# Kernel tuning notes

Measured on AMD Instinct MI355X. Metric: run time of the kernel, lower is better.

## Reference

```python
import jax, jax.numpy as jnp
import numpy as np

B, S, D_MODEL, D_POL = 2048, 64, 768, 64
SCALE = 1.0 / np.sqrt(D_POL).astype(np.float32)  # 1/sqrt(policy_d) = 0.125


def mish(x):
    return x * jnp.tanh(jax.nn.softplus(x))


def setup_inputs() -> dict:
    key = jax.random.key(0)
    ks = jax.random.split(key, 10)
    s = lambda fan: 1.0 / np.sqrt(fan)
    return {
        "x": jax.random.normal(ks[0], (B, S, D_MODEL), dtype=jnp.float32),
        "W1": jax.random.normal(ks[1], (D_MODEL, D_MODEL), dtype=jnp.float32) * s(D_MODEL),
        "b1": jax.random.normal(ks[2], (D_MODEL,), dtype=jnp.float32) * 0.01,
        "Wq": jax.random.normal(ks[3], (D_MODEL, D_POL), dtype=jnp.float32) * s(D_MODEL),
        "bq": jax.random.normal(ks[4], (D_POL,), dtype=jnp.float32) * 0.01,
        "Wk": jax.random.normal(ks[5], (D_MODEL, D_POL), dtype=jnp.float32) * s(D_MODEL),
        "bk": jax.random.normal(ks[6], (D_POL,), dtype=jnp.float32) * 0.01,
        "Wp": jax.random.normal(ks[7], (D_POL, 4), dtype=jnp.float32) * s(D_POL),
        "bp": jax.random.normal(ks[8], (4,), dtype=jnp.float32) * 0.01,
        "indices": jax.random.randint(ks[9], (1858,), 0, 4288, dtype=jnp.int64 if jax.config.read("jax_enable_x64") else jnp.int32),
    }


def reference(x, W1, b1, Wq, bq, Wk, bk, Wp, bp, indices):
    b = x.shape[0]
    h = mish(x @ W1 + b1)                      # [B,64,768] dense1 + mish
    q = h @ Wq + bq                            # [B,64,64]
    k = h @ Wk + bk                            # [B,64,64]
    scores = jnp.einsum("bqd,bkd->bqk", q, k) * SCALE  # [B,64,64]
    # promotion head on 8th-rank keys: Linear(D_POL -> 4)
    prom = k[:, 56:64, :] @ Wp + bp            # [B,8,4]
    # transpose/split[3,1]/add/transpose == add 4th channel to first 3
    prom = prom[:, :, :3] + prom[:, :, 3:4]    # [B,8,3]
    prom = prom.reshape(b, 1, 24)
    s2 = scores[:, 48:56, 56:64].reshape(b, 64, 1)
    s2 = jnp.concatenate([s2, s2, s2], axis=-1).reshape(b, 8, 24)
    promotion = (s2 + prom).reshape(b, 3, 64)  # [B,3,64]
    policy = jnp.concatenate([scores, promotion], axis=1).reshape(b, 4288)
    return policy[:, indices]                  # [B,1858]
```

## Files before the change

### kernel.cpp

```cpp
#include <hip/hip_runtime.h>

typedef __attribute__((ext_vector_type(8))) short short8;
typedef __attribute__((ext_vector_type(4))) float f32x4;
typedef __attribute__((ext_vector_type(4))) short short4v;

#define DM 768
#define DP 64

__device__ __forceinline__ unsigned short f2bf(float f) {
  unsigned u = __float_as_uint(f);
  u = u + 0x7fffu + ((u >> 16) & 1u);
  return (unsigned short)(u >> 16);
}
__device__ __forceinline__ float bf2f(unsigned short s) {
  return __uint_as_float(((unsigned)s) << 16);
}
__device__ __forceinline__ float mishf(float v) {
  float t = __expf(fminf(v, 30.0f));
  float num = t * (t + 2.0f);
  return v * (num / (num + 2.0f));
}

__global__ void cvt_frag(const float* __restrict__ src, unsigned short* __restrict__ dst,
                         int N, int ntPer) {
  constexpr int MAXC = 192;
  constexpr int TS = MAXC + 8;
  __shared__ unsigned short tile[32 * TS];
  const int kt = blockIdx.x;
  const int nt0 = blockIdx.y * ntPer;
  const int cols = ntPer * 16;
  for (int e = threadIdx.x; e < 32 * cols; e += blockDim.x) {
    int row = e / cols, col = e - row * cols;
    tile[row * TS + col] = f2bf(src[(kt * 32 + row) * N + nt0 * 16 + col]);
  }
  __syncthreads();
  const int NT = N / 16;
  for (int s = threadIdx.x; s < ntPer * 64; s += blockDim.x) {
    int ntl = s >> 6, l = s & 63;
    int m16 = l & 15, quad = l >> 4;
    short8 v;
    #pragma unroll
    for (int j = 0; j < 8; ++j)
      v[j] = (short)tile[(quad * 8 + j) * TS + ntl * 16 + m16];
    *(short8*)(dst + ((size_t)((kt * NT + nt0 + ntl) * 64 + l)) * 8) = v;
  }
}

__global__ __launch_bounds__(1024, 4) void fused_policy(
    const float* __restrict__ x, const float* __restrict__ b1,
    const float* __restrict__ bq, const float* __restrict__ bk,
    const float* __restrict__ Wp, const float* __restrict__ bp,
    const int* __restrict__ idxs, int n_idx,
    const unsigned short* __restrict__ W1f,
    const unsigned short* __restrict__ Wqf,
    const unsigned short* __restrict__ Wkf,
    float* __restrict__ out) {
  constexpr int XS  = 136;
  constexpr int HSS = 776;
  constexpr int QKS = 72;

  __shared__ __align__(16) unsigned char smemA[64 * HSS * 2];
  __shared__ __align__(16) unsigned short qkbuf[4][64 * QKS];
  __shared__ float promf[32];

  unsigned short* hs  = (unsigned short*)smemA;
  unsigned short* xs0 = (unsigned short*)smemA;
  unsigned short* xs1 = xs0 + 64 * XS;
  float* sc = (float*)smemA;
  unsigned short* qsh = qkbuf[0];
  unsigned short* qsl = qkbuf[1];
  unsigned short* ksh = qkbuf[2];
  unsigned short* ksl = qkbuf[3];

  const int b    = blockIdx.x;
  const int tid  = threadIdx.x;
  const int wave = tid >> 6;
  const int lane = tid & 63;
  const int m16  = lane & 15;
  const int quad = lane >> 4;

  const float* xb = x + (size_t)b * (64 * DM);

  f32x4 acc[4][3];
  #pragma unroll
  for (int rt = 0; rt < 4; ++rt)
    #pragma unroll
    for (int ct = 0; ct < 3; ++ct)
      #pragma unroll
      for (int r = 0; r < 4; ++r) acc[rt][ct][r] = 0.0f;

  float b1v[3];
  #pragma unroll
  for (int ct = 0; ct < 3; ++ct) b1v[ct] = b1[wave * 48 + ct * 16 + m16];

  const unsigned short* wb = W1f + ((size_t)(wave * 3) * 64 + lane) * 8;
  short8 bcur[3], bnxt[3];
  #pragma unroll
  for (int ct = 0; ct < 3; ++ct) bcur[ct] = *(const short8*)(wb + ct * 512);

  float4 pv0, pv1;
  {
    int e0 = tid, e1 = tid + 1024;
    pv0 = *(const float4*)(xb + (e0 >> 5) * DM + (e0 & 31) * 4);
    pv1 = *(const float4*)(xb + (e1 >> 5) * DM + (e1 & 31) * 4);
  }

  for (int c = 0; c < 6; ++c) {
    unsigned short* xw = (c & 1) ? xs1 : xs0;
    {
      int e0 = tid, e1 = tid + 1024;
      short4v s4;
      s4.x = (short)f2bf(pv0.x); s4.y = (short)f2bf(pv0.y);
      s4.z = (short)f2bf(pv0.z); s4.w = (short)f2bf(pv0.w);
      *(short4v*)(xw + (e0 >> 5) * XS + (e0 & 31) * 4) = s4;
      s4.x = (short)f2bf(pv1.x); s4.y = (short)f2bf(pv1.y);
      s4.z = (short)f2bf(pv1.z); s4.w = (short)f2bf(pv1.w);
      *(short4v*)(xw + (e1 >> 5) * XS + (e1 & 31) * 4) = s4;
    }
    __syncthreads();
    if (c < 5) {
      int kb = (c + 1) * 128;
      int e0 = tid, e1 = tid + 1024;
      pv0 = *(const float4*)(xb + (e0 >> 5) * DM + kb + (e0 & 31) * 4);
      pv1 = *(const float4*)(xb + (e1 >> 5) * DM + kb + (e1 & 31) * 4);
    }
    #pragma unroll
    for (int ks = 0; ks < 4; ++ks) {
      const int kt = c * 4 + ks;
      short8 af[4];
      #pragma unroll
      for (int rt = 0; rt < 4; ++rt)
        af[rt] = *(const short8*)(xw + (rt * 16 + m16) * XS + ks * 32 + quad * 8);
      if (kt < 23) {
        #pragma unroll
        for (int ct = 0; ct < 3; ++ct)
          bnxt[ct] = *(const short8*)(wb + (kt + 1) * 24576 + ct * 512);
      }
      #pragma unroll
      for (int rt = 0; rt < 4; ++rt)
        #pragma unroll
        for (int ct = 0; ct < 3; ++ct)
          acc[rt][ct] = __builtin_amdgcn_mfma_f32_16x16x32_bf16(af[rt], bcur[ct], acc[rt][ct], 0, 0, 0);
      if (kt < 23) {
        #pragma unroll
        for (int ct = 0; ct < 3; ++ct) bcur[ct] = bnxt[ct];
      }
    }
  }
  __syncthreads();

  #pragma unroll
  for (int rt = 0; rt < 4; ++rt)
    #pragma unroll
    for (int ct = 0; ct < 3; ++ct)
      #pragma unroll
      for (int r = 0; r < 4; ++r) {
        int row = rt * 16 + quad * 4 + r;
        int col = wave * 48 + ct * 16 + m16;
        hs[row * HSS + col] = f2bf(mishf(acc[rt][ct][r] + b1v[ct]));
      }
  __syncthreads();

  {
    const int grp = wave >> 3;
    const int w8 = wave & 7;
    const int rt = w8 & 3;
    const int ch = w8 >> 2;
    const unsigned short* Wf = grp ? Wkf : Wqf;
    const float* bias = grp ? bk : bq;
    unsigned short* oh = grp ? ksh : qsh;
    unsigned short* ol = grp ? ksl : qsl;

    f32x4 acc2[2];
    #pragma unroll
    for (int ct2 = 0; ct2 < 2; ++ct2)
      #pragma unroll
      for (int r = 0; r < 4; ++r) acc2[ct2][r] = 0.0f;

    const unsigned short* wfb = Wf + ((size_t)(ch * 2) * 64 + lane) * 8;
    short8 c2[2], n2[2];
    #pragma unroll
    for (int ct2 = 0; ct2 < 2; ++ct2) c2[ct2] = *(const short8*)(wfb + ct2 * 512);

    const int arow = (rt * 16 + m16) * HSS;
    short8 a = *(const short8*)(hs + arow + quad * 8);
    for (int kt = 0; kt < 24; ++kt) {
      short8 an;
      if (kt < 23) {
        an = *(const short8*)(hs + arow + (kt + 1) * 32 + quad * 8);
        #pragma unroll
        for (int ct2 = 0; ct2 < 2; ++ct2)
          n2[ct2] = *(const short8*)(wfb + (kt + 1) * 2048 + ct2 * 512);
      }
      #pragma unroll
      for (int ct2 = 0; ct2 < 2; ++ct2)
        acc2[ct2] = __builtin_amdgcn_mfma_f32_16x16x32_bf16(a, c2[ct2], acc2[ct2], 0, 0, 0);
      if (kt < 23) {
        a = an;
        #pragma unroll
        for (int ct2 = 0; ct2 < 2; ++ct2) c2[ct2] = n2[ct2];
      }
    }
    #pragma unroll
    for (int ct2 = 0; ct2 < 2; ++ct2)
      #pragma unroll
      for (int r = 0; r < 4; ++r) {
        int row = rt * 16 + quad * 4 + r;
        int col = ch * 32 + ct2 * 16 + m16;
        float v = acc2[ct2][r] + bias[col];
        unsigned short vh = f2bf(v);
        unsigned short vl = f2bf(v - bf2f(vh));
        oh[row * QKS + col] = vh;
        ol[row * QKS + col] = vl;
      }
  }
  __syncthreads();

  {
    const int rt = wave >> 2, ctt = wave & 3;
    f32x4 a3;
    #pragma unroll
    for (int r = 0; r < 4; ++r) a3[r] = 0.0f;
    #pragma unroll
    for (int kt = 0; kt < 2; ++kt) {
      const int k0 = kt * 32;
      short8 ah = *(const short8*)(qsh + (rt * 16 + m16) * QKS + k0 + quad * 8);
      short8 al = *(const short8*)(qsl + (rt * 16 + m16) * QKS + k0 + quad * 8);
      short8 bh = *(const short8*)(ksh + (ctt * 16 + m16) * QKS + k0 + quad * 8);
      short8 bl = *(const short8*)(ksl + (ctt * 16 + m16) * QKS + k0 + quad * 8);
      a3 = __builtin_amdgcn_mfma_f32_16x16x32_bf16(ah, bh, a3, 0, 0, 0);
      a3 = __builtin_amdgcn_mfma_f32_16x16x32_bf16(ah, bl, a3, 0, 0, 0);
      a3 = __builtin_amdgcn_mfma_f32_16x16x32_bf16(al, bh, a3, 0, 0, 0);
    }
    #pragma unroll
    for (int r = 0; r < 4; ++r)
      sc[(rt * 16 + quad * 4 + r) * 64 + ctt * 16 + m16] = a3[r] * 0.125f;

    if (wave == 15 && lane < 32) {
      const int rr = lane >> 2;
      const int c = lane & 3;
      float s = bp[c];
      const int krow = (56 + rr) * QKS;
      #pragma unroll
      for (int d = 0; d < 64; ++d) {
        float kv = bf2f(ksh[krow + d]) + bf2f(ksl[krow + d]);
        s += kv * Wp[d * 4 + c];
      }
      promf[lane] = s;
    }
  }
  __syncthreads();

  float* outb = out + (size_t)b * n_idx;
  for (int i = tid; i < n_idx; i += 1024) {
    int idx = idxs[i];
    float v;
    if (idx < 4096) {
      v = sc[idx];
    } else {
      int f = idx - 4096;
      int r = f / 24;
      int j = f - r * 24;
      int jj = j / 3;
      int cc = j - jj * 3;
      v = sc[(48 + r) * 64 + 56 + jj] + promf[jj * 4 + cc] + promf[jj * 4 + 3];
    }
    outb[i] = v;
  }
}

extern "C" void kernel_launch(void* const* d_in, const int* in_sizes, int n_in,
                              void* d_out, int out_size, void* d_ws, size_t ws_size,
                              hipStream_t stream) {
  const float* x  = (const float*)d_in[0];
  const float* W1 = (const float*)d_in[1];
  const float* b1 = (const float*)d_in[2];
  const float* Wq = (const float*)d_in[3];
  const float* bq = (const float*)d_in[4];
  const float* Wk = (const float*)d_in[5];
  const float* bk = (const float*)d_in[6];
  const float* Wp = (const float*)d_in[7];
  const float* bp = (const float*)d_in[8];
  const int* idxs = (const int*)d_in[9];

  const int B = in_sizes[0] / (64 * DM);
  const int n_idx = in_sizes[9];

  unsigned short* W1f = (unsigned short*)d_ws;
  unsigned short* Wqf = W1f + 768 * 768;
  unsigned short* Wkf = Wqf + 64 * 768;

  cvt_frag<<<dim3(24, 4), 256, 0, stream>>>(W1, W1f, 768, 12);
  cvt_frag<<<dim3(24, 1), 256, 0, stream>>>(Wq, Wqf, 64, 4);
  cvt_frag<<<dim3(24, 1), 256, 0, stream>>>(Wk, Wkf, 64, 4);

  fused_policy<<<B, 1024, 0, stream>>>(x, b1, bq, bk, Wp, bp, idxs, n_idx,
                                       W1f, Wqf, Wkf, (float*)d_out);
}
```

Before: 770.4 us.

## Split dense1 into two 32-row halves to shrink LDS and registers

Dense1 and the Q/K projection now run in two passes over 32-row halves of the 64 tokens instead of one pass over all 64. This halves the accumulator registers and shrinks shared memory from about 116KB to 80KB. Padded LDS strides are replaced with XOR swizzles to avoid bank conflicts, and the launch-bound occupancy hint is raised from 4 to 8. The intent is to lower register and LDS pressure per block, at the cost of extra barriers and a re-read of the W1 fragments for each half.

```diff
diff --git a/kernel.cpp b/kernel.cpp
--- a/kernel.cpp
+++ b/kernel.cpp
@@ -46,7 +46,7 @@
   }
 }
 
-__global__ __launch_bounds__(1024, 4) void fused_policy(
+__global__ __launch_bounds__(1024, 8) void fused_policy(
     const float* __restrict__ x, const float* __restrict__ b1,
     const float* __restrict__ bq, const float* __restrict__ bk,
     const float* __restrict__ Wp, const float* __restrict__ bp,
@@ -55,22 +55,18 @@
     const unsigned short* __restrict__ Wqf,
     const unsigned short* __restrict__ Wkf,
     float* __restrict__ out) {
-  constexpr int XS  = 136;
-  constexpr int HSS = 776;
-  constexpr int QKS = 72;
-
-  __shared__ __align__(16) unsigned char smemA[64 * HSS * 2];
-  __shared__ __align__(16) unsigned short qkbuf[4][64 * QKS];
-  __shared__ float promf[32];
-
-  unsigned short* hs  = (unsigned short*)smemA;
-  unsigned short* xs0 = (unsigned short*)smemA;
-  unsigned short* xs1 = xs0 + 64 * XS;
-  float* sc = (float*)smemA;
-  unsigned short* qsh = qkbuf[0];
-  unsigned short* qsl = qkbuf[1];
-  unsigned short* ksh = qkbuf[2];
-  unsigned short* ksl = qkbuf[3];
+  constexpr int XS = 136;
+
+  __shared__ __align__(16) unsigned char smem[81920];
+  unsigned short* xs0 = (unsigned short*)smem;
+  unsigned short* xs1 = (unsigned short*)(smem + 8704);
+  unsigned short* hs  = (unsigned short*)smem;
+  float* sc           = (float*)smem;
+  float* promf        = (float*)(smem + 16384);
+  unsigned short* qsh = (unsigned short*)(smem + 49152);
+  unsigned short* qsl = (unsigned short*)(smem + 49152 + 8192);
+  unsigned short* ksh = (unsigned short*)(smem + 49152 + 16384);
+  unsigned short* ksl = (unsigned short*)(smem + 49152 + 24576);
 
   const int b    = blockIdx.x;
   const int tid  = threadIdx.x;
@@ -81,153 +77,130 @@
 
   const float* xb = x + (size_t)b * (64 * DM);
 
-  f32x4 acc[4][3];
-  #pragma unroll
-  for (int rt = 0; rt < 4; ++rt)
-    #pragma unroll
-    for (int ct = 0; ct < 3; ++ct)
-      #pragma unroll
-      for (int r = 0; r < 4; ++r) acc[rt][ct][r] = 0.0f;
-
   float b1v[3];
   #pragma unroll
   for (int ct = 0; ct < 3; ++ct) b1v[ct] = b1[wave * 48 + ct * 16 + m16];
 
   const unsigned short* wb = W1f + ((size_t)(wave * 3) * 64 + lane) * 8;
-  short8 bcur[3], bnxt[3];
-  #pragma unroll
-  for (int ct = 0; ct < 3; ++ct) bcur[ct] = *(const short8*)(wb + ct * 512);
-
-  float4 pv0, pv1;
-  {
-    int e0 = tid, e1 = tid + 1024;
-    pv0 = *(const float4*)(xb + (e0 >> 5) * DM + (e0 & 31) * 4);
-    pv1 = *(const float4*)(xb + (e1 >> 5) * DM + (e1 & 31) * 4);
-  }
-
-  for (int c = 0; c < 6; ++c) {
-    unsigned short* xw = (c & 1) ? xs1 : xs0;
+
+  const int grp  = wave >> 3;
+  const int w8   = wave & 7;
+  const int rtl2 = w8 >> 2;
+  const int ct2w = w8 & 3;
+  const unsigned short* Wf = grp ? Wkf : Wqf;
+  const float* bias2 = grp ? bk : bq;
+  unsigned short* oh = grp ? ksh : qsh;
+  unsigned short* ol = grp ? ksl : qsl;
+  const unsigned short* wfb = Wf + ((size_t)ct2w * 64 + lane) * 8;
+
+  float4 pv = *(const float4*)(xb + (tid >> 5) * DM + (tid & 31) * 4);
+
+  for (int half = 0; half < 2; ++half) {
+    const float* xh = xb + half * 32 * DM;
+
+    f32x4 acc[2][3];
+    #pragma unroll
+    for (int rtl = 0; rtl < 2; ++rtl)
+      #pragma unroll
+      for (int ct = 0; ct < 3; ++ct)
+        #pragma unroll
+        for (int r = 0; r < 4; ++r) acc[rtl][ct][r] = 0.0f;
+
+    short8 bcur[3];
+    #pragma unroll
+    for (int ct = 0; ct < 3; ++ct) bcur[ct] = *(const short8*)(wb + ct * 512);
+
+    for (int c = 0; c < 6; ++c) {
+      unsigned short* xw = (c & 1) ? xs1 : xs0;
+      {
+        short4v s4;
+        s4.x = (short)f2bf(pv.x); s4.y = (short)f2bf(pv.y);
+        s4.z = (short)f2bf(pv.z); s4.w = (short)f2bf(pv.w);
+        *(short4v*)(xw + (tid >> 5) * XS + (tid & 31) * 4) = s4;
+      }
+      __syncthreads();
+      if (c < 5)
+        pv = *(const float4*)(xh + (tid >> 5) * DM + (c + 1) * 128 + (tid & 31) * 4);
+      #pragma unroll
+      for (int ks = 0; ks < 4; ++ks) {
+        const int kt = c * 4 + ks;
+        short8 af0 = *(const short8*)(xw + m16 * XS + ks * 32 + quad * 8);
+        short8 af1 = *(const short8*)(xw + (16 + m16) * XS + ks * 32 + quad * 8);
+        #pragma unroll
+        for (int ct = 0; ct < 3; ++ct) {
+          short8 bn;
+          if (kt < 23) bn = *(const short8*)(wb + (kt + 1) * 24576 + ct * 512);
+          acc[0][ct] = __builtin_amdgcn_mfma_f32_16x16x32_bf16(af0, bcur[ct], acc[0][ct], 0, 0, 0);
+          acc[1][ct] = __builtin_amdgcn_mfma_f32_16x16x32_bf16(af1, bcur[ct], acc[1][ct], 0, 0, 0);
+          if (kt < 23) bcur[ct] = bn;
+        }
+      }
+    }
+    __syncthreads();
+
+    if (half == 0)
+      pv = *(const float4*)(xb + 32 * DM + (tid >> 5) * DM + (tid & 31) * 4);
+
+    #pragma unroll
+    for (int rtl = 0; rtl < 2; ++rtl)
+      #pragma unroll
+      for (int ct = 0; ct < 3; ++ct)
+        #pragma unroll
+        for (int r = 0; r < 4; ++r) {
+          int row = rtl * 16 + quad * 4 + r;
+          int col = wave * 48 + ct * 16 + m16;
+          hs[row * 768 + (col ^ ((row & 15) << 3))] = f2bf(mishf(acc[rtl][ct][r] + b1v[ct]));
+        }
+    __syncthreads();
+
     {
-      int e0 = tid, e1 = tid + 1024;
-      short4v s4;
-      s4.x = (short)f2bf(pv0.x); s4.y = (short)f2bf(pv0.y);
-      s4.z = (short)f2bf(pv0.z); s4.w = (short)f2bf(pv0.w);
-      *(short4v*)(xw + (e0 >> 5) * XS + (e0 & 31) * 4) = s4;
-      s4.x = (short)f2bf(pv1.x); s4.y = (short)f2bf(pv1.y);
-      s4.z = (short)f2bf(pv1.z); s4.w = (short)f2bf(pv1.w);
-      *(short4v*)(xw + (e1 >> 5) * XS + (e1 & 31) * 4) = s4;
-    }
-    __syncthreads();
-    if (c < 5) {
-      int kb = (c + 1) * 128;
-      int e0 = tid, e1 = tid + 1024;
-      pv0 = *(const float4*)(xb + (e0 >> 5) * DM + kb + (e0 & 31) * 4);
-      pv1 = *(const float4*)(xb + (e1 >> 5) * DM + kb + (e1 & 31) * 4);
-    }
-    #pragma unroll
-    for (int ks = 0; ks < 4; ++ks) {
-      const int kt = c * 4 + ks;
-      short8 af[4];
-      #pragma unroll
-      for (int rt = 0; rt < 4; ++rt)
-        af[rt] = *(const short8*)(xw + (rt * 16 + m16) * XS + ks * 32 + quad * 8);
-      if (kt < 23) {
-        #pragma unroll
-        for (int ct = 0; ct < 3; ++ct)
-          bnxt[ct] = *(const short8*)(wb + (kt + 1) * 24576 + ct * 512);
-      }
-      #pragma unroll
-      for (int rt = 0; rt < 4; ++rt)
-        #pragma unroll
-        for (int ct = 0; ct < 3; ++ct)
-          acc[rt][ct] = __builtin_amdgcn_mfma_f32_16x16x32_bf16(af[rt], bcur[ct], acc[rt][ct], 0, 0, 0);
-      if (kt < 23) {
-        #pragma unroll
-        for (int ct = 0; ct < 3; ++ct) bcur[ct] = bnxt[ct];
-      }
-    }
-  }
-  __syncthreads();
-
-  #pragma unroll
-  for (int rt = 0; rt < 4; ++rt)
-    #pragma unroll
-    for (int ct = 0; ct < 3; ++ct)
+      f32x4 a2;
+      #pragma unroll
+      for (int r = 0; r < 4; ++r) a2[r] = 0.0f;
+
+      const int arow = rtl2 * 16 + m16;
+      const unsigned short* hrow = hs + arow * 768;
+      const int swz = m16 << 3;
+
+      short8 a = *(const short8*)(hrow + ((quad * 8) ^ swz));
+      short8 bf0 = *(const short8*)(wfb);
+      for (int kt = 0; kt < 24; ++kt) {
+        short8 an, bn;
+        if (kt < 23) {
+          an = *(const short8*)(hrow + (((kt + 1) * 32 + quad * 8) ^ swz));
+          bn = *(const short8*)(wfb + (kt + 1) * 2048);
+        }
+        a2 = __builtin_amdgcn_mfma_f32_16x16x32_bf16(a, bf0, a2, 0, 0, 0);
+        if (kt < 23) { a = an; bf0 = bn; }
+      }
       #pragma unroll
       for (int r = 0; r < 4; ++r) {
-        int row = rt * 16 + quad * 4 + r;
-        int col = wave * 48 + ct * 16 + m16;
-        hs[row * HSS + col] = f2bf(mishf(acc[rt][ct][r] + b1v[ct]));
-      }
-  __syncthreads();
-
-  {
-    const int grp = wave >> 3;
-    const int w8 = wave & 7;
-    const int rt = w8 & 3;
-    const int ch = w8 >> 2;
-    const unsigned short* Wf = grp ? Wkf : Wqf;
-    const float* bias = grp ? bk : bq;
-    unsigned short* oh = grp ? ksh : qsh;
-    unsigned short* ol = grp ? ksl : qsl;
-
-    f32x4 acc2[2];
-    #pragma unroll
-    for (int ct2 = 0; ct2 < 2; ++ct2)
-      #pragma unroll
-      for (int r = 0; r < 4; ++r) acc2[ct2][r] = 0.0f;
-
-    const unsigned short* wfb = Wf + ((size_t)(ch * 2) * 64 + lane) * 8;
-    short8 c2[2], n2[2];
-    #pragma unroll
-    for (int ct2 = 0; ct2 < 2; ++ct2) c2[ct2] = *(const short8*)(wfb + ct2 * 512);
-
-    const int arow = (rt * 16 + m16) * HSS;
-    short8 a = *(const short8*)(hs + arow + quad * 8);
-    for (int kt = 0; kt < 24; ++kt) {
-      short8 an;
-      if (kt < 23) {
-        an = *(const short8*)(hs + arow + (kt + 1) * 32 + quad * 8);
-        #pragma unroll
-        for (int ct2 = 0; ct2 < 2; ++ct2)
-          n2[ct2] = *(const short8*)(wfb + (kt + 1) * 2048 + ct2 * 512);
-      }
-      #pragma unroll
-      for (int ct2 = 0; ct2 < 2; ++ct2)
-        acc2[ct2] = __builtin_amdgcn_mfma_f32_16x16x32_bf16(a, c2[ct2], acc2[ct2], 0, 0, 0);
-      if (kt < 23) {
-        a = an;
-        #pragma unroll
-        for (int ct2 = 0; ct2 < 2; ++ct2) c2[ct2] = n2[ct2];
-      }
-    }
-    #pragma unroll
-    for (int ct2 = 0; ct2 < 2; ++ct2)
-      #pragma unroll
-      for (int r = 0; r < 4; ++r) {
-        int row = rt * 16 + quad * 4 + r;
-        int col = ch * 32 + ct2 * 16 + m16;
-        float v = acc2[ct2][r] + bias[col];
+        int rowg = half * 32 + rtl2 * 16 + quad * 4 + r;
+        int col = ct2w * 16 + m16;
+        float v = a2[r] + bias2[col];
         unsigned short vh = f2bf(v);
         unsigned short vl = f2bf(v - bf2f(vh));
-        oh[row * QKS + col] = vh;
-        ol[row * QKS + col] = vl;
-      }
-  }
-  __syncthreads();
+        int qi = rowg * 64 + (col ^ ((rowg & 7) << 3));
+        oh[qi] = vh; ol[qi] = vl;
+      }
+    }
+    __syncthreads();
+  }
 
   {
     const int rt = wave >> 2, ctt = wave & 3;
     f32x4 a3;
     #pragma unroll
     for (int r = 0; r < 4; ++r) a3[r] = 0.0f;
+    const int qrow = rt * 16 + m16, krow = ctt * 16 + m16;
+    const int sq = (qrow & 7) << 3, sk = (krow & 7) << 3;
     #pragma unroll
     for (int kt = 0; kt < 2; ++kt) {
-      const int k0 = kt * 32;
-      short8 ah = *(const short8*)(qsh + (rt * 16 + m16) * QKS + k0 + quad * 8);
-      short8 al = *(const short8*)(qsl + (rt * 16 + m16) * QKS + k0 + quad * 8);
-      short8 bh = *(const short8*)(ksh + (ctt * 16 + m16) * QKS + k0 + quad * 8);
-      short8 bl = *(const short8*)(ksl + (ctt * 16 + m16) * QKS + k0 + quad * 8);
+      const int k0 = kt * 32 + quad * 8;
+      short8 ah = *(const short8*)(qsh + qrow * 64 + (k0 ^ sq));
+      short8 al = *(const short8*)(qsl + qrow * 64 + (k0 ^ sq));
+      short8 bh = *(const short8*)(ksh + krow * 64 + (k0 ^ sk));
+      short8 bl = *(const short8*)(ksl + krow * 64 + (k0 ^ sk));
       a3 = __builtin_amdgcn_mfma_f32_16x16x32_bf16(ah, bh, a3, 0, 0, 0);
       a3 = __builtin_amdgcn_mfma_f32_16x16x32_bf16(ah, bl, a3, 0, 0, 0);
       a3 = __builtin_amdgcn_mfma_f32_16x16x32_bf16(al, bh, a3, 0, 0, 0);
@@ -240,10 +213,12 @@
       const int rr = lane >> 2;
       const int c = lane & 3;
       float s = bp[c];
-      const int krow = (56 + rr) * QKS;
+      const int krow2 = 56 + rr;
+      const int swzk = rr << 3;
       #pragma unroll
       for (int d = 0; d < 64; ++d) {
-        float kv = bf2f(ksh[krow + d]) + bf2f(ksl[krow + d]);
+        int ki = krow2 * 64 + (d ^ swzk);
+        float kv = bf2f(ksh[ki]) + bf2f(ksl[ki]);
         s += kv * Wp[d * 4 + c];
       }
       promf[lane] = s;
```

Measured after the change: 3.011 ms. +290.9%, slower.
